# Kernel tuning notes

Hardware: AMD Instinct MI355X
Metric: run time of the kernel (lower is better)

## Reference

```python
import jax, jax.numpy as jnp
import numpy as np


def setup_inputs() -> dict:
    key = jax.random.key(0)
    ks = jax.random.split(key, 8)
    B, N, K, C_in, M, C_add, C_out = 2, 40000, 16, 64, 16, 3, 128
    in_features = (C_in + C_add) * M  # 1072
    input_features = jax.random.normal(ks[0], (B, N, C_in), dtype=jnp.float32)
    neighbor_inds = jax.random.randint(ks[1], (B, N, K), 0, N, dtype=jnp.int64)
    inverse_neighbors = jax.random.randint(ks[2], (B, N * K), 0, N * K, dtype=jnp.int64)
    inverse_k = jax.random.randint(ks[3], (B, N * K), 0, K, dtype=jnp.int64)
    inverse_idx = jax.random.randint(ks[4], (B, N * K), 0, N, dtype=jnp.int64)
    weightnet = jax.random.normal(ks[5], (B, N, K, M), dtype=jnp.float32)
    additional_features = jax.random.normal(ks[6], (B, N, K, C_add), dtype=jnp.float32)
    bound = 1.0 / np.sqrt(in_features)
    kw, kb = jax.random.split(ks[7])
    linear_weight = jax.random.uniform(kw, (C_out, in_features), dtype=jnp.float32, minval=-bound, maxval=bound)
    linear_bias = jax.random.uniform(kb, (C_out,), dtype=jnp.float32, minval=-bound, maxval=bound)
    return {
        "input_features": input_features,
        "neighbor_inds": neighbor_inds,
        "inverse_neighbors": inverse_neighbors,
        "inverse_k": inverse_k,
        "inverse_idx": inverse_idx,
        "weightnet": weightnet,
        "additional_features": additional_features,
        "linear_weight": linear_weight,
        "linear_bias": linear_bias,
    }


def reference(input_features, neighbor_inds, inverse_neighbors, inverse_k, inverse_idx,
              weightnet, additional_features, linear_weight, linear_bias):
    # inverse_* tensors are only used by the custom CUDA backward; unused here.
    B, N, K = neighbor_inds.shape
    # gather neighbor features: [B, N, K, C_in]
    gathered = jnp.take_along_axis(input_features[:, :, None, :],
                                   neighbor_inds[..., None], axis=1)
    # concat extra per-neighbor features -> [B, N, K, C]
    feats = jnp.concatenate([gathered, additional_features], axis=-1)
    # PConv: [B,N,C,K] @ [B,N,K,M] -> [B,N,C,M] -> flatten to [B,N,C*M]
    pconv = jnp.einsum('bnkc,bnkm->bncm', feats, weightnet)
    pconv = pconv.reshape(B, N, -1)
    # fused linear
    out = jnp.einsum('bnf,of->bno', pconv, linear_weight) + linear_bias
    return out
```

## Files before the change

### kernel.cpp

```cpp
#include <hip/hip_runtime.h>
#include <stdint.h>

typedef unsigned short u16;
typedef short short8 __attribute__((ext_vector_type(8)));
typedef float floatx4 __attribute__((ext_vector_type(4)));

#define NPERB   40000
#define NPTS    80000
#define KNBR    16
#define CIN     64
#define MDIM    16
#define CADD    3
#define CF      (CIN + CADD)
#define COUT    128
#define KF      1072
#define KP      1088
#define NKT     34
#define PTSB    32
#define SLAB    129

__device__ __forceinline__ u16 f2bf(float f) {
    union { float f; unsigned int u; } v; v.f = f;
    unsigned int u = v.u;
    return (u16)((u + 0x7FFFu + ((u >> 16) & 1u)) >> 16);
}
__device__ __forceinline__ short8 pack8(floatx4 x, floatx4 y) {
    union { short8 v; u16 a[8]; } u;
    u.a[0] = f2bf(x[0]); u.a[1] = f2bf(x[1]); u.a[2] = f2bf(x[2]); u.a[3] = f2bf(x[3]);
    u.a[4] = f2bf(y[0]); u.a[5] = f2bf(y[1]); u.a[6] = f2bf(y[2]); u.a[7] = f2bf(y[3]);
    return u.v;
}
__device__ __forceinline__ unsigned swz(unsigned chunk) {
    return chunk ^ ((chunk >> 3) & 7u);
}

__global__ void prep_lw_kernel(const float* __restrict__ lw, u16* __restrict__ lwp) {
    int i = blockIdx.x * 256 + threadIdx.x;
    if (i >= COUT * KP) return;
    int o = i / KP, f = i - o * KP;
    lwp[i] = (f < KF) ? f2bf(lw[(size_t)o * KF + f]) : (u16)0;
}

__global__ __launch_bounds__(512) void fused_kernel(
    const float* __restrict__ inp,
    const int*   __restrict__ nbr,
    const float* __restrict__ wn,
    const float* __restrict__ addl,
    const u16*   __restrict__ lwp,
    const float* __restrict__ bias,
    float* __restrict__ out)
{
    __shared__ __align__(16) u16 Apc[(NKT * SLAB + 8) * 8];

    const int wave = threadIdx.x >> 6;
    const int lane = threadIdx.x & 63;
    const int pbase = blockIdx.x * PTSB;
    const float* inpb = inp + ((pbase >= NPERB) ? (size_t)NPERB * CIN : 0);

    const int em = lane & 15, ec = lane >> 4;
    for (int i = 0; i < PTSB / 8; i++) {
        const int pr = wave * 4 + i;
        const int p  = __builtin_amdgcn_readfirstlane(pbase + pr);
        const float* wp  = wn  + (size_t)p * (KNBR * MDIM);
        const int*  nbrp = nbr + (size_t)p * KNBR;

        float av_hold = (lane < KNBR * CADD)
                          ? addl[(size_t)p * (KNBR * CADD) + lane] : 0.f;

        float wv[KNBR];
#pragma unroll
        for (int k = 0; k < KNBR; k++) wv[k] = wp[k * MDIM + em];

        {
            float ev = 0.f;
#pragma unroll
            for (int k = 0; k < KNBR; k++)
                ev += __shfl(av_hold, k * CADD + ec) * wv[k];
            if (ec == 3) ev = 0.f;
            unsigned kt   = 32 + (lane >> 5);
            unsigned quad = (lane >> 3) & 3;
            unsigned ch   = kt * SLAB + (unsigned)pr * 4 + quad;
            Apc[swz(ch) * 8 + (lane & 7)] = f2bf(ev);
        }

        const floatx4* wp4 = (const floatx4*)wp;
        floatx4 a0 = 0, a1 = 0, a2 = 0, a3 = 0;
#pragma unroll
        for (int k = 0; k < KNBR; k++) {
            int idx = nbrp[k];
            float fv = inpb[(size_t)idx * CIN + lane];
            floatx4 w0 = wp4[k * 4 + 0];
            floatx4 w1 = wp4[k * 4 + 1];
            floatx4 w2 = wp4[k * 4 + 2];
            floatx4 w3 = wp4[k * 4 + 3];
            a0 += fv * w0; a1 += fv * w1; a2 += fv * w2; a3 += fv * w3;
        }
        {
            unsigned kt = lane >> 1, qb = (lane & 1) * 2;
            unsigned ch = kt * SLAB + (unsigned)pr * 4 + qb;
            *(short8*)&Apc[swz(ch) * 8]     = pack8(a0, a1);
            *(short8*)&Apc[swz(ch + 1) * 8] = pack8(a2, a3);
        }
    }
    __syncthreads();

    const int r16 = lane & 15, quad = lane >> 4;
    const int rt = wave & 1;
    const int c0 = (wave >> 1) * 32;
    const u16* B0p = lwp + (size_t)(c0 + r16) * KP + quad * 8;
    const u16* B1p = B0p + (size_t)16 * KP;
    const unsigned abase = (unsigned)(rt * 16 + r16) * 4 + quad;

    floatx4 acc0 = 0, acc1 = 0;
#pragma unroll 2
    for (int kt = 0; kt < NKT; kt++) {
        short8 A  = *(const short8*)&Apc[swz((unsigned)kt * SLAB + abase) * 8];
        short8 B0 = *(const short8*)(B0p + kt * 32);
        short8 B1 = *(const short8*)(B1p + kt * 32);
        acc0 = __builtin_amdgcn_mfma_f32_16x16x32_bf16(A, B0, acc0, 0, 0, 0);
        acc1 = __builtin_amdgcn_mfma_f32_16x16x32_bf16(A, B1, acc1, 0, 0, 0);
    }

    const float bv0 = bias[c0 + r16];
    const float bv1 = bias[c0 + 16 + r16];
#pragma unroll
    for (int r = 0; r < 4; r++) {
        const size_t row = (size_t)(pbase + rt * 16 + quad * 4 + r) * COUT;
        out[row + c0 + r16]      = acc0[r] + bv0;
        out[row + c0 + 16 + r16] = acc1[r] + bv1;
    }
}

__global__ __launch_bounds__(256) void fused_fallback_kernel(
    const float* __restrict__ inp, const int* __restrict__ nbr,
    const float* __restrict__ wn, const float* __restrict__ addl,
    const float* __restrict__ lw, const float* __restrict__ bias,
    float* __restrict__ out)
{
    const int p = blockIdx.x;
    const int b = p / NPERB;
    const int tid = threadIdx.x;
    __shared__ float sf[KNBR * CF];
    __shared__ float sw[KNBR * MDIM];
    __shared__ float sp[KF];

    sw[tid] = wn[(size_t)p * (KNBR * MDIM) + tid];
    for (int i = tid; i < KNBR * CIN; i += 256) {
        int k = i >> 6, c = i & 63;
        int idx = nbr[(size_t)p * KNBR + k];
        sf[k * CF + c] = inp[((size_t)b * NPERB + idx) * CIN + c];
    }
    if (tid < KNBR * CADD) {
        int k = tid / CADD, c = tid - k * CADD;
        sf[k * CF + CIN + c] = addl[(size_t)p * (KNBR * CADD) + tid];
    }
    __syncthreads();
    for (int f = tid; f < KF; f += 256) {
        int c = f >> 4, m = f & 15;
        float s = 0;
#pragma unroll
        for (int k = 0; k < KNBR; k++) s += sf[k * CF + c] * sw[k * MDIM + m];
        sp[f] = s;
    }
    __syncthreads();
    const int o = tid >> 1, h = tid & 1;
    float s = 0;
    for (int f = h * (KF / 2); f < (h + 1) * (KF / 2); f++)
        s += sp[f] * lw[(size_t)o * KF + f];
    s += __shfl_xor(s, 1);
    if (h == 0) out[(size_t)p * COUT + o] = s + bias[o];
}

extern "C" void kernel_launch(void* const* d_in, const int* in_sizes, int n_in,
                              void* d_out, int out_size, void* d_ws, size_t ws_size,
                              hipStream_t stream) {
    const float* inp  = (const float*)d_in[0];
    const int*   nbr  = (const int*)d_in[1];
    const float* wn   = (const float*)d_in[5];
    const float* addl = (const float*)d_in[6];
    const float* lw   = (const float*)d_in[7];
    const float* bias = (const float*)d_in[8];
    float* out = (float*)d_out;

    const size_t lw_bytes = (size_t)COUT * KP * sizeof(u16);
    if (ws_size < lw_bytes) {
        fused_fallback_kernel<<<NPTS, 256, 0, stream>>>(inp, nbr, wn, addl, lw, bias, out);
        return;
    }
    u16* lwp = (u16*)d_ws;
    prep_lw_kernel<<<(COUT * KP + 255) / 256, 256, 0, stream>>>(lw, lwp);
    fused_kernel<<<NPTS / PTSB, 512, 0, stream>>>(inp, nbr, wn, addl, lwp, bias, out);
}
```

Measured before the change: 357.5 us.

## Halve points per block and batch all gathers with async weightnet LDS loads

Each block now handles 16 points, with each wave processing two points. All 32 neighbor indices and gathered features are issued up front behind a single waitcnt, and weightnet is loaded directly into LDS with global_load_lds. The aim is to expose more memory-level parallelism in the latency-bound gather phase and raise occupancy through a smaller LDS footprint and a launch-bounds hint. The tradeoff is twice as many blocks, each re-reading the linear weight, with only one MFMA tile per wave and much higher register pressure from the held feature arrays.

```diff
diff --git a/kernel.cpp b/kernel.cpp
--- a/kernel.cpp
+++ b/kernel.cpp
@@ -16,8 +16,8 @@
 #define KF      1072
 #define KP      1088
 #define NKT     34
-#define PTSB    32
-#define SLAB    129
+#define PTSB    16
+#define SLAB    65
 
 __device__ __forceinline__ u16 f2bf(float f) {
     union { float f; unsigned int u; } v; v.f = f;
@@ -33,6 +33,11 @@
 __device__ __forceinline__ unsigned swz(unsigned chunk) {
     return chunk ^ ((chunk >> 3) & 7u);
 }
+__device__ __forceinline__ void gload_lds16(const void* g, void* l) {
+    __builtin_amdgcn_global_load_lds(
+        (const __attribute__((address_space(1))) void*)g,
+        (__attribute__((address_space(3))) void*)l, 16, 0, 0);
+}
 
 __global__ void prep_lw_kernel(const float* __restrict__ lw, u16* __restrict__ lwp) {
     int i = blockIdx.x * 256 + threadIdx.x;
@@ -41,7 +46,39 @@
     lwp[i] = (f < KF) ? f2bf(lw[(size_t)o * KF + f]) : (u16)0;
 }
 
-__global__ __launch_bounds__(512) void fused_kernel(
+__device__ __forceinline__ void compute_point(
+    int pr, int lane, float av, const float (&fv)[KNBR],
+    const float* wl, u16* Apc)
+{
+    const int em = lane & 15, ec = lane >> 4;
+    float ev = 0.f;
+#pragma unroll
+    for (int k = 0; k < KNBR; k++)
+        ev += __shfl(av, k * CADD + ec) * wl[k * MDIM + em];
+    if (ec == 3) ev = 0.f;
+    {
+        unsigned kt   = 32 + (lane >> 5);
+        unsigned quad = (lane >> 3) & 3;
+        unsigned ch   = kt * SLAB + (unsigned)pr * 4 + quad;
+        Apc[swz(ch) * 8 + (lane & 7)] = f2bf(ev);
+    }
+    floatx4 a0 = 0, a1 = 0, a2 = 0, a3 = 0;
+#pragma unroll
+    for (int k = 0; k < KNBR; k++) {
+        const floatx4* w4 = (const floatx4*)(wl + k * MDIM);
+        const float fvk = fv[k];
+        a0 += fvk * w4[0]; a1 += fvk * w4[1];
+        a2 += fvk * w4[2]; a3 += fvk * w4[3];
+    }
+    {
+        unsigned kt = lane >> 1, qb = (lane & 1) * 2;
+        unsigned ch = kt * SLAB + (unsigned)pr * 4 + qb;
+        *(short8*)&Apc[swz(ch) * 8]     = pack8(a0, a1);
+        *(short8*)&Apc[swz(ch + 1) * 8] = pack8(a2, a3);
+    }
+}
+
+__global__ __launch_bounds__(512, 6) void fused_kernel(
     const float* __restrict__ inp,
     const int*   __restrict__ nbr,
     const float* __restrict__ wn,
@@ -50,84 +87,66 @@
     const float* __restrict__ bias,
     float* __restrict__ out)
 {
-    __shared__ __align__(16) u16 Apc[(NKT * SLAB + 8) * 8];
+    __shared__ __align__(16) u16   Apc[(NKT * SLAB + 8) * 8];
+    __shared__ __align__(16) float Wns[PTSB * KNBR * MDIM];
 
     const int wave = threadIdx.x >> 6;
     const int lane = threadIdx.x & 63;
     const int pbase = blockIdx.x * PTSB;
     const float* inpb = inp + ((pbase >= NPERB) ? (size_t)NPERB * CIN : 0);
 
-    const int em = lane & 15, ec = lane >> 4;
-    for (int i = 0; i < PTSB / 8; i++) {
-        const int pr = wave * 4 + i;
-        const int p  = __builtin_amdgcn_readfirstlane(pbase + pr);
-        const float* wp  = wn  + (size_t)p * (KNBR * MDIM);
-        const int*  nbrp = nbr + (size_t)p * KNBR;
-
-        float av_hold = (lane < KNBR * CADD)
-                          ? addl[(size_t)p * (KNBR * CADD) + lane] : 0.f;
-
-        float wv[KNBR];
-#pragma unroll
-        for (int k = 0; k < KNBR; k++) wv[k] = wp[k * MDIM + em];
-
-        {
-            float ev = 0.f;
-#pragma unroll
-            for (int k = 0; k < KNBR; k++)
-                ev += __shfl(av_hold, k * CADD + ec) * wv[k];
-            if (ec == 3) ev = 0.f;
-            unsigned kt   = 32 + (lane >> 5);
-            unsigned quad = (lane >> 3) & 3;
-            unsigned ch   = kt * SLAB + (unsigned)pr * 4 + quad;
-            Apc[swz(ch) * 8 + (lane & 7)] = f2bf(ev);
-        }
-
-        const floatx4* wp4 = (const floatx4*)wp;
-        floatx4 a0 = 0, a1 = 0, a2 = 0, a3 = 0;
-#pragma unroll
-        for (int k = 0; k < KNBR; k++) {
-            int idx = nbrp[k];
-            float fv = inpb[(size_t)idx * CIN + lane];
-            floatx4 w0 = wp4[k * 4 + 0];
-            floatx4 w1 = wp4[k * 4 + 1];
-            floatx4 w2 = wp4[k * 4 + 2];
-            floatx4 w3 = wp4[k * 4 + 3];
-            a0 += fv * w0; a1 += fv * w1; a2 += fv * w2; a3 += fv * w3;
-        }
-        {
-            unsigned kt = lane >> 1, qb = (lane & 1) * 2;
-            unsigned ch = kt * SLAB + (unsigned)pr * 4 + qb;
-            *(short8*)&Apc[swz(ch) * 8]     = pack8(a0, a1);
-            *(short8*)&Apc[swz(ch + 1) * 8] = pack8(a2, a3);
-        }
-    }
+    const int pr0 = wave * 2;
+    const int p0  = __builtin_amdgcn_readfirstlane(pbase + pr0);
+    const int p1  = p0 + 1;
+
+    float* wl0 = Wns + pr0 * (KNBR * MDIM);
+    float* wl1 = wl0 + KNBR * MDIM;
+    gload_lds16(wn + (size_t)p0 * (KNBR * MDIM) + lane * 4, wl0);
+    gload_lds16(wn + (size_t)p1 * (KNBR * MDIM) + lane * 4, wl1);
+
+    float av0 = (lane < KNBR * CADD) ? addl[(size_t)p0 * (KNBR * CADD) + lane] : 0.f;
+    float av1 = (lane < KNBR * CADD) ? addl[(size_t)p1 * (KNBR * CADD) + lane] : 0.f;
+
+    const int* nb0 = nbr + (size_t)p0 * KNBR;
+    const int* nb1 = nbr + (size_t)p1 * KNBR;
+    int idx0[KNBR], idx1[KNBR];
+#pragma unroll
+    for (int k = 0; k < KNBR; k++) idx0[k] = nb0[k];
+#pragma unroll
+    for (int k = 0; k < KNBR; k++) idx1[k] = nb1[k];
+
+    float fv0[KNBR], fv1[KNBR];
+#pragma unroll
+    for (int k = 0; k < KNBR; k++) fv0[k] = inpb[(size_t)idx0[k] * CIN + lane];
+#pragma unroll
+    for (int k = 0; k < KNBR; k++) fv1[k] = inpb[(size_t)idx1[k] * CIN + lane];
+
+    asm volatile("s_waitcnt vmcnt(0)" ::: "memory");
+    __builtin_amdgcn_sched_barrier(0);
+
+    compute_point(pr0,     lane, av0, fv0, wl0, Apc);
+    compute_point(pr0 + 1, lane, av1, fv1, wl1, Apc);
+
+    const int r16 = lane & 15, quad = lane >> 4;
+    const int c0 = wave * 16;
+    const u16* Bp = lwp + (size_t)(c0 + r16) * KP + quad * 8;
+    const unsigned abase = (unsigned)r16 * 4 + quad;
+    const float bv = bias[c0 + r16];
+
     __syncthreads();
 
-    const int r16 = lane & 15, quad = lane >> 4;
-    const int rt = wave & 1;
-    const int c0 = (wave >> 1) * 32;
-    const u16* B0p = lwp + (size_t)(c0 + r16) * KP + quad * 8;
-    const u16* B1p = B0p + (size_t)16 * KP;
-    const unsigned abase = (unsigned)(rt * 16 + r16) * 4 + quad;
-
-    floatx4 acc0 = 0, acc1 = 0;
+    floatx4 acc = 0;
 #pragma unroll 2
     for (int kt = 0; kt < NKT; kt++) {
-        short8 A  = *(const short8*)&Apc[swz((unsigned)kt * SLAB + abase) * 8];
-        short8 B0 = *(const short8*)(B0p + kt * 32);
-        short8 B1 = *(const short8*)(B1p + kt * 32);
-        acc0 = __builtin_amdgcn_mfma_f32_16x16x32_bf16(A, B0, acc0, 0, 0, 0);
-        acc1 = __builtin_amdgcn_mfma_f32_16x16x32_bf16(A, B1, acc1, 0, 0, 0);
-    }
-
-    const float bv0 = bias[c0 + r16];
-    const float bv1 = bias[c0 + 16 + r16];
+        short8 A = *(const short8*)&Apc[swz((unsigned)kt * SLAB + abase) * 8];
+        short8 B = *(const short8*)(Bp + kt * 32);
+        acc = __builtin_amdgcn_mfma_f32_16x16x32_bf16(A, B, acc, 0, 0, 0);
+    }
+
 #pragma unroll
     for (int r = 0; r < 4; r++) {
-        const size_t row = (size_t)(pbase + rt * 16 + quad * 4 + r) * COUT;
-        out[row + c0 + r16]      = acc0[r] + bv0;
-        out[row + c0 + 16 + r16] = acc1[r] + bv1;
+        const size_t row = (size_t)(pbase + quad * 4 + r) * COUT;
+        out[row + c0 + r16] = acc[r] + bv;
     }
 }
 
```

New measurement: 378.0 us. +5.7%, slower.
